# Optimization experiments

Hardware: AMD Instinct MI355X
Metric: run time of the kernel (lower is better)

Reference implementation:

```python
import jax, jax.numpy as jnp
import numpy as np

NUM_TREES = 150
ARITY = 4
DEPTH = 4
NUM_LEVELS = DEPTH + 1  # leaves (level 0) ... root (level DEPTH)
VOCAB = 10000
SUBTOK = 8
EMB_DIM = 256
HID = 256
NUM_CLASSES = 2


def _build_forest():
    # perfect ARITY-ary tree, level-order indexing; edges point child -> parent
    n = (ARITY ** (DEPTH + 1) - 1) // (ARITY - 1)  # 341
    src = np.arange(1, n)
    dst = (src - 1) // ARITY
    depth_of = np.zeros(n, dtype=np.int64)
    for j in range(1, n):
        depth_of[j] = depth_of[(j - 1) // ARITY] + 1
    level_of = DEPTH - depth_of  # leaves = 0, processed first (topo order)
    offs = np.arange(NUM_TREES) * n
    edge_src = (src[None, :] + offs[:, None]).ravel().astype(np.int32)
    edge_dst = (dst[None, :] + offs[:, None]).ravel().astype(np.int32)
    node_level = np.tile(level_of, NUM_TREES).astype(np.int32)
    graph_id = np.repeat(np.arange(NUM_TREES), n).astype(np.int32)
    leaf_mask = (node_level == 0).astype(np.int32)
    return edge_src, edge_dst, node_level, graph_id, leaf_mask, NUM_TREES * n


def setup_inputs() -> dict:
    key = jax.random.key(0)
    ks = jax.random.split(key, 16)
    es, ed, lvl, gid, lm, N = _build_forest()
    s_e = 1.0 / np.sqrt(EMB_DIM)
    s_h = 1.0 / np.sqrt(HID)
    s_f = 1.0 / np.sqrt(2 * HID)
    return {
        "node_feat1": jax.random.randint(ks[0], (N, SUBTOK), 0, VOCAB, dtype=jnp.int32),
        "node_feat2": jax.random.randint(ks[1], (N, SUBTOK), 0, VOCAB, dtype=jnp.int32),
        "emb1": jax.random.normal(ks[2], (VOCAB, EMB_DIM), jnp.float32) * 0.02,
        "emb2": jax.random.normal(ks[3], (VOCAB, EMB_DIM), jnp.float32) * 0.02,
        "W_iou1": jax.random.normal(ks[4], (EMB_DIM, 3 * HID), jnp.float32) * s_e,
        "W_iou2": jax.random.normal(ks[5], (EMB_DIM, 3 * HID), jnp.float32) * s_e,
        "U_iou1": jax.random.normal(ks[6], (HID, 3 * HID), jnp.float32) * s_h,
        "U_iou2": jax.random.normal(ks[7], (HID, 3 * HID), jnp.float32) * s_h,
        "Uf_W1": jax.random.normal(ks[8], (HID, HID), jnp.float32) * s_h,
        "Uf_b1": jnp.zeros((HID,), jnp.float32),
        "Uf_W2": jax.random.normal(ks[9], (HID, HID), jnp.float32) * s_h,
        "Uf_b2": jnp.zeros((HID,), jnp.float32),
        "b_iou1": jnp.zeros((3 * HID,), jnp.float32),
        "b_iou2": jnp.zeros((3 * HID,), jnp.float32),
        "Wf": jax.random.normal(ks[10], (2 * HID, NUM_CLASSES), jnp.float32) * s_f,
        "bf": jnp.zeros((NUM_CLASSES,), jnp.float32),
        "edge_src": jnp.asarray(es),
        "edge_dst": jnp.asarray(ed),
        "node_level": jnp.asarray(lvl),
        "graph_id": jnp.asarray(gid),
        "leaf_mask": jnp.asarray(lm),
    }


def _tree_lstm(iou0, U_iou, Uf_W, Uf_b, b_iou, edge_src, edge_dst, node_level):
    # ChildSum TreeLSTM, propagated level-by-level (leaves -> root)
    N = iou0.shape[0]
    h = jnp.zeros((N, HID), iou0.dtype)
    c = jnp.zeros((N, HID), iou0.dtype)
    for lvl in range(NUM_LEVELS):
        emask = (node_level[edge_dst] == lvl).astype(h.dtype)[:, None]  # [E,1]
        hs = h[edge_src] * emask  # children h (already computed at lower levels)
        f = jax.nn.sigmoid(hs @ Uf_W + Uf_b)  # per-edge forget gate
        h_tild = jax.ops.segment_sum(hs, edge_dst, num_segments=N)
        c_sum = jax.ops.segment_sum(f * c[edge_src] * emask, edge_dst, num_segments=N)
        has_child = jax.ops.segment_sum(emask, edge_dst, num_segments=N) > 0  # [N,1]
        # DGL semantics: reduce overwrites iou for internal nodes; leaves keep W_iou(x)*mask
        iou = jnp.where(has_child, h_tild @ U_iou, iou0) + b_iou
        i, o, u = jnp.split(iou, 3, axis=1)
        c_new = jax.nn.sigmoid(i) * jnp.tanh(u) + c_sum
        h_new = jax.nn.sigmoid(o) * jnp.tanh(c_new)
        at = (node_level == lvl)[:, None]
        h = jnp.where(at, h_new, h)
        c = jnp.where(at, c_new, c)
    return h


def _branch(node_feat, emb, W_iou, U_iou, Uf_W, Uf_b, b_iou,
            leaf_mask, edge_src, edge_dst, node_level, graph_id):
    embeds = emb[node_feat].mean(axis=1)  # subtoken mean pooling -> [N, EMB_DIM]
    iou0 = (embeds @ W_iou) * leaf_mask.astype(embeds.dtype)[:, None]
    h = _tree_lstm(iou0, U_iou, Uf_W, Uf_b, b_iou, edge_src, edge_dst, node_level)
    s = jax.ops.segment_sum(h, graph_id, num_segments=NUM_TREES)
    cnt = jax.ops.segment_sum(jnp.ones((h.shape[0],), h.dtype), graph_id, num_segments=NUM_TREES)
    return jax.nn.relu(s / cnt[:, None])  # mean graph readout + relu


def reference(node_feat1, node_feat2, emb1, emb2, W_iou1, W_iou2, U_iou1, U_iou2,
              Uf_W1, Uf_b1, Uf_W2, Uf_b2, b_iou1, b_iou2, Wf, bf,
              edge_src, edge_dst, node_level, graph_id, leaf_mask):
    m1 = _branch(node_feat1, emb1, W_iou1, U_iou1, Uf_W1, Uf_b1, b_iou1,
                 leaf_mask, edge_src, edge_dst, node_level, graph_id)
    m2 = _branch(node_feat2, emb2, W_iou2, U_iou2, Uf_W2, Uf_b2, b_iou2,
                 leaf_mask, edge_src, edge_dst, node_level, graph_id)
    logits = jax.nn.leaky_relu(jnp.concatenate([m1, m2], axis=1) @ Wf + bf, 0.01)
    return jax.nn.softmax(logits, axis=-1)
```

## Files before the change

kernel.cpp:

```cpp
#include <hip/hip_runtime.h>

#define NT 150
#define NPT 341
#define LEAF0 85
#define NL (NT*256)
#define NN (NT*NPT)
#define VOCAB 10000

typedef __attribute__((ext_vector_type(8))) short short8;
typedef __attribute__((ext_vector_type(4))) float floatx4;

__device__ __forceinline__ float sigf(float x){
  return __builtin_amdgcn_rcpf(1.0f + __expf(-x));
}
__device__ __forceinline__ float tanh_fast(float x){
  float e = __expf(2.0f*x);
  return 1.0f - 2.0f*__builtin_amdgcn_rcpf(e + 1.0f);
}
__device__ __forceinline__ float bf2f(ushort u){ union{unsigned i; float f;} v; v.i = ((unsigned)u)<<16; return v.f; }
__device__ __forceinline__ ushort f2bf(float x){ union{float f; unsigned i;} v; v.f = x; return (ushort)((v.i + 0x7fff + ((v.i>>16)&1))>>16); }

__global__ __launch_bounds__(256) void prep_k(
    const float* __restrict__ e1, const float* __restrict__ e2,
    ushort* __restrict__ E1, ushort* __restrict__ E2,
    const float* __restrict__ W1, const float* __restrict__ U1, const float* __restrict__ F1,
    const float* __restrict__ W2, const float* __restrict__ U2, const float* __restrict__ F2,
    ushort* Wt1, ushort* Ut1, ushort* Ft1, ushort* Wt2, ushort* Ut2, ushort* Ft2){
  __shared__ float T[32][33];
  int bid = blockIdx.x;
  if (bid < 5000){
    const float* s = (bid >= 2500) ? e2 : e1;
    ushort* d = (bid >= 2500) ? E2 : E1;
    size_t i = ((size_t)(bid % 2500)*256 + threadIdx.x)*4;
    float4 v = *(const float4*)&s[i];
    d[i+0]=f2bf(v.x); d[i+1]=f2bf(v.y); d[i+2]=f2bf(v.z); d[i+3]=f2bf(v.w);
    return;
  }
  int w = bid - 5000;
  int z = w / 192, rem = w % 192;
  int bx = rem % 24, by = rem / 24;
  const float* src; ushort* dst; int N;
  switch (z){
    case 0: src=W1; dst=Wt1; N=768; break;
    case 1: src=U1; dst=Ut1; N=768; break;
    case 2: src=F1; dst=Ft1; N=256; break;
    case 3: src=W2; dst=Wt2; N=768; break;
    case 4: src=U2; dst=Ut2; N=768; break;
    default: src=F2; dst=Ft2; N=256; break;
  }
  int n0 = bx*32; if (n0 >= N) return;
  int k0 = by*32;
  int nl = threadIdx.x & 31, kb = threadIdx.x >> 5;
  #pragma unroll
  for (int i=0;i<4;i++){ int kk = kb*4+i; T[kk][nl] = src[(size_t)(k0+kk)*N + n0 + nl]; }
  __syncthreads();
  #pragma unroll
  for (int i=0;i<4;i++){ int nn = kb*4+i; dst[(size_t)(n0+nn)*256 + k0 + nl] = f2bf(T[nl][nn]); }
}

__global__ __launch_bounds__(1024) void leaf_gemm(
    const int* __restrict__ f1, const int* __restrict__ f2,
    const ushort* __restrict__ E1, const ushort* __restrict__ E2,
    const ushort* __restrict__ Wt1, const float* __restrict__ b1,
    const ushort* __restrict__ Wt2, const float* __restrict__ b2,
    ushort* __restrict__ h1, ushort* __restrict__ c1,
    ushort* __restrict__ h2, ushort* __restrict__ c2){
  __shared__ __attribute__((aligned(16))) ushort As[8][64*40];
  int br = blockIdx.y;
  const int* feat = br ? f2 : f1;
  const ushort* E = br ? E2 : E1;
  const ushort* Wt = br ? Wt2 : Wt1;
  const float* biou = br ? b2 : b1;
  ushort* h = br ? h2 : h1;
  ushort* c = br ? c2 : c1;
  int tid = threadIdx.x;
  int lane = tid & 63, wav = tid >> 6, quad = lane >> 4, l15 = lane & 15;
  int rowbase = blockIdx.x*64;

  {
    int row = tid >> 4, seg = tid & 15;
    int leaf = rowbase + row;
    int tree = leaf >> 8;
    size_t node = (size_t)tree*NPT + LEAF0 + (leaf & 255);
    const int* f = feat + node*8;
    float s[16];
    #pragma unroll
    for (int q=0;q<16;q++) s[q]=0.f;
    #pragma unroll
    for (int j=0;j<8;j++){
      const ushort* rowp = E + (size_t)f[j]*256 + seg*16;
      short8 a = *(const short8*)rowp;
      short8 b = *(const short8*)(rowp+8);
      #pragma unroll
      for (int q=0;q<8;q++){ s[q]+=bf2f((ushort)a[q]); s[8+q]+=bf2f((ushort)b[q]); }
    }
    short8 o1, o2;
    #pragma unroll
    for (int q=0;q<8;q++){ o1[q]=(short)f2bf(s[q]*0.125f); o2[q]=(short)f2bf(s[8+q]*0.125f); }
    int cch = seg >> 1, off = (seg & 1)*16;
    *(short8*)&As[cch][row*40 + off]     = o1;
    *(short8*)&As[cch][row*40 + off + 8] = o2;
  }
  __syncthreads();

  floatx4 acc[3][4];
  #pragma unroll
  for (int g=0;g<3;g++)
    #pragma unroll
    for (int r=0;r<4;r++) acc[g][r] = (floatx4){0.f,0.f,0.f,0.f};

  const ushort* bp0 = Wt + (size_t)(0*256 + wav*16 + l15)*256 + quad*8;
  const ushort* bp1 = Wt + (size_t)(1*256 + wav*16 + l15)*256 + quad*8;
  const ushort* bp2 = Wt + (size_t)(2*256 + wav*16 + l15)*256 + quad*8;

  #pragma unroll
  for (int cch=0; cch<8; cch++){
    short8 b0 = *(const short8*)(bp0 + cch*32);
    short8 b1 = *(const short8*)(bp1 + cch*32);
    short8 b2 = *(const short8*)(bp2 + cch*32);
    #pragma unroll
    for (int r=0;r<4;r++){
      short8 a = *(const short8*)&As[cch][(16*r + l15)*40 + quad*8];
      acc[0][r] = __builtin_amdgcn_mfma_f32_16x16x32_bf16(a, b0, acc[0][r], 0,0,0);
      acc[1][r] = __builtin_amdgcn_mfma_f32_16x16x32_bf16(a, b1, acc[1][r], 0,0,0);
      acc[2][r] = __builtin_amdgcn_mfma_f32_16x16x32_bf16(a, b2, acc[2][r], 0,0,0);
    }
  }
  int hc = wav*16 + l15;
  float bi = biou[hc], bo = biou[256+hc], bu = biou[512+hc];
  #pragma unroll
  for (int r=0;r<4;r++){
    #pragma unroll
    for (int reg=0;reg<4;reg++){
      int leaf = rowbase + 16*r + quad*4 + reg;
      int tree = leaf >> 8;
      size_t node = (size_t)tree*NPT + LEAF0 + (leaf & 255);
      float iv = acc[0][r][reg] + bi;
      float ov = acc[1][r][reg] + bo;
      float uv = acc[2][r][reg] + bu;
      float cc = sigf(iv)*tanh_fast(uv);
      float hh = sigf(ov)*tanh_fast(cc);
      h[node*256 + hc] = f2bf(hh);
      c[node*256 + hc] = f2bf(cc);
    }
  }
}

__global__ __launch_bounds__(256) void level_k(
    const ushort* __restrict__ Ut1, const ushort* __restrict__ Ft1,
    const float* __restrict__ Ufb1, const float* __restrict__ bi1,
    const ushort* __restrict__ Ut2, const ushort* __restrict__ Ft2,
    const float* __restrict__ Ufb2, const float* __restrict__ bi2,
    ushort* __restrict__ h1, ushort* __restrict__ c1,
    ushort* __restrict__ h2, ushort* __restrict__ c2,
    int M, int shift, int base){
  __shared__ __attribute__((aligned(16))) ushort Ch[8][64*40];
  int br = blockIdx.z;
  const ushort* Ut = br ? Ut2 : Ut1;
  const ushort* Ft = br ? Ft2 : Ft1;
  const float* Ufb = br ? Ufb2 : Ufb1;
  const float* biou = br ? bi2 : bi1;
  ushort* h = br ? h2 : h1;
  ushort* c = br ? c2 : c1;
  int tid = threadIdx.x;
  int lane = tid & 63, wav = tid >> 6, quad = lane >> 4, l15 = lane & 15;
  int m0 = blockIdx.x*16, cb = blockIdx.y;
  int mask = (1<<shift)-1;

  {
    int cl = tid >> 2, q4 = tid & 3;
    int sm = m0 + (cl >> 2); if (sm > M-1) sm = M-1;
    int stree = sm >> shift, sloc = base + (sm & mask);
    const ushort* sgp = h + ((size_t)stree*NPT + 4*sloc + 1 + (cl & 3))*256 + q4*8;
    #pragma unroll
    for (int cc=0;cc<8;cc++)
      *(short8*)&Ch[cc][cl*40 + q4*8] = *(const short8*)(sgp + cc*32);
  }
  __syncthreads();

  int col = cb*64 + wav*16 + l15;
  const ushort* bfp = Ft + (size_t)col*256 + quad*8;
  const ushort* bp0 = Ut + (size_t)(0*256 + col)*256 + quad*8;
  const ushort* bp1 = Ut + (size_t)(256 + col)*256 + quad*8;
  const ushort* bp2 = Ut + (size_t)(512 + col)*256 + quad*8;

  floatx4 af[4], ai[4], ao[4], au[4];
  #pragma unroll
  for (int r=0;r<4;r++){
    af[r] = (floatx4){0.f,0.f,0.f,0.f}; ai[r] = (floatx4){0.f,0.f,0.f,0.f};
    ao[r] = (floatx4){0.f,0.f,0.f,0.f}; au[r] = (floatx4){0.f,0.f,0.f,0.f};
  }

  #pragma unroll
  for (int cc=0; cc<8; cc++){
    short8 Bf = *(const short8*)(bfp + cc*32);
    short8 Bi = *(const short8*)(bp0 + cc*32);
    short8 Bo = *(const short8*)(bp1 + cc*32);
    short8 Bu = *(const short8*)(bp2 + cc*32);
    #pragma unroll
    for (int r=0;r<4;r++){
      short8 a = *(const short8*)&Ch[cc][(16*r + l15)*40 + quad*8];
      af[r] = __builtin_amdgcn_mfma_f32_16x16x32_bf16(a, Bf, af[r], 0,0,0);
      ai[r] = __builtin_amdgcn_mfma_f32_16x16x32_bf16(a, Bi, ai[r], 0,0,0);
      ao[r] = __builtin_amdgcn_mfma_f32_16x16x32_bf16(a, Bo, ao[r], 0,0,0);
      au[r] = __builtin_amdgcn_mfma_f32_16x16x32_bf16(a, Bu, au[r], 0,0,0);
    }
  }

  float ufb = Ufb[col];
  float bI = biou[col], bO = biou[256+col], bU = biou[512+col];
  #pragma unroll
  for (int r=0;r<4;r++){
    int m = m0 + 4*r + quad;
    int mm = m < M ? m : M-1;
    int tree = mm >> shift, loc = base + (mm & mask);
    size_t ch0 = ((size_t)tree*NPT + 4*loc + 1)*256 + col;
    float cs = 0.f;
    #pragma unroll
    for (int reg=0;reg<4;reg++)
      cs += sigf(af[r][reg] + ufb) * bf2f(c[ch0 + (size_t)reg*256]);
    float iv = ai[r][0]+ai[r][1]+ai[r][2]+ai[r][3] + bI;
    float ov = ao[r][0]+ao[r][1]+ao[r][2]+ao[r][3] + bO;
    float uv = au[r][0]+au[r][1]+au[r][2]+au[r][3] + bU;
    float cn = sigf(iv)*tanh_fast(uv) + cs;
    float hn = sigf(ov)*tanh_fast(cn);
    if (m < M){
      size_t off = ((size_t)tree*NPT + loc)*256 + col;
      h[off] = f2bf(hn);
      c[off] = f2bf(cn);
    }
  }
}

__global__ __launch_bounds__(256) void readout_k(
    const ushort* __restrict__ h1, const ushort* __restrict__ h2,
    float* __restrict__ mp1, float* __restrict__ mp2){
  __shared__ float red[4][256];
  int br = blockIdx.z, part = blockIdx.y, tree = blockIdx.x;
  const ushort* h = br ? h2 : h1;
  float* mp = br ? mp2 : mp1;
  int t = threadIdx.x;
  int lane = t & 63, rg = t >> 6;
  int start = part*85;
  int cnt = (part==3) ? 86 : 85;
  const ushort* base = h + ((size_t)tree*NPT + start)*256 + lane*4;
  float s0=0.f,s1=0.f,s2=0.f,s3=0.f;
  for (int i=rg; i<cnt; i+=4){
    ushort4 v = *(const ushort4*)(base + (size_t)i*256);
    s0 += bf2f(v.x); s1 += bf2f(v.y); s2 += bf2f(v.z); s3 += bf2f(v.w);
  }
  *(float4*)&red[rg][lane*4] = make_float4(s0,s1,s2,s3);
  __syncthreads();
  float tot = red[0][t]+red[1][t]+red[2][t]+red[3][t];
  mp[((size_t)tree*4 + part)*256 + t] = tot;
}

__global__ __launch_bounds__(64) void final_k(const float* __restrict__ mp1,
    const float* __restrict__ mp2, const float* __restrict__ Wf,
    const float* __restrict__ bf, float* __restrict__ out){
  int tree = blockIdx.x; int t = threadIdx.x;
  float p0=0.f, p1=0.f;
  for (int k=t;k<512;k+=64){
    const float* mp = (k<256) ? mp1 : mp2;
    int kk = k & 255;
    size_t b0 = ((size_t)tree*4)*256 + kk;
    float s = mp[b0] + mp[b0+256] + mp[b0+512] + mp[b0+768];
    float x = fmaxf(s*(1.0f/341.0f), 0.f);
    p0 += x*Wf[k*2+0]; p1 += x*Wf[k*2+1];
  }
  #pragma unroll
  for (int off=32; off>0; off>>=1){
    p0 += __shfl_down(p0, off);
    p1 += __shfl_down(p1, off);
  }
  if (t==0){
    float l0 = p0+bf[0], l1 = p1+bf[1];
    l0 = (l0>0.f)?l0:0.01f*l0;
    l1 = (l1>0.f)?l1:0.01f*l1;
    float mx = fmaxf(l0,l1);
    float e0 = __expf(l0-mx), e1 = __expf(l1-mx);
    float inv = 1.0f/(e0+e1);
    out[tree*2+0] = e0*inv; out[tree*2+1] = e1*inv;
  }
}

extern "C" void kernel_launch(void* const* d_in, const int* in_sizes, int n_in,
                              void* d_out, int out_size, void* d_ws, size_t ws_size,
                              hipStream_t stream) {
  const int*   feat1 = (const int*)  d_in[0];
  const int*   feat2 = (const int*)  d_in[1];
  const float* emb1  = (const float*)d_in[2];
  const float* emb2  = (const float*)d_in[3];
  const float* Wiou1 = (const float*)d_in[4];
  const float* Wiou2 = (const float*)d_in[5];
  const float* Uiou1 = (const float*)d_in[6];
  const float* Uiou2 = (const float*)d_in[7];
  const float* UfW1  = (const float*)d_in[8];
  const float* Ufb1  = (const float*)d_in[9];
  const float* UfW2  = (const float*)d_in[10];
  const float* Ufb2  = (const float*)d_in[11];
  const float* biou1 = (const float*)d_in[12];
  const float* biou2 = (const float*)d_in[13];
  const float* Wf    = (const float*)d_in[14];
  const float* bfv   = (const float*)d_in[15];
  float* out = (float*)d_out;

  char* ws = (char*)d_ws;
  ushort* h1  = (ushort*)ws;  ws += (size_t)NN*256*2;
  ushort* h2  = (ushort*)ws;  ws += (size_t)NN*256*2;
  ushort* c1  = (ushort*)ws;  ws += (size_t)NN*256*2;
  ushort* c2  = (ushort*)ws;  ws += (size_t)NN*256*2;
  ushort* E1  = (ushort*)ws;  ws += (size_t)VOCAB*256*2;
  ushort* E2  = (ushort*)ws;  ws += (size_t)VOCAB*256*2;
  ushort* Wt1 = (ushort*)ws;  ws += 768*256*2;
  ushort* Ut1 = (ushort*)ws;  ws += 768*256*2;
  ushort* Ft1 = (ushort*)ws;  ws += 256*256*2;
  ushort* Wt2 = (ushort*)ws;  ws += 768*256*2;
  ushort* Ut2 = (ushort*)ws;  ws += 768*256*2;
  ushort* Ft2 = (ushort*)ws;  ws += 256*256*2;
  float*  mp1 = (float*)ws;   ws += (size_t)NT*4*256*4;
  float*  mp2 = (float*)ws;   ws += (size_t)NT*4*256*4;

  prep_k<<<dim3(6152), 256, 0, stream>>>(emb1, emb2, E1, E2,
                                         Wiou1, Uiou1, UfW1, Wiou2, Uiou2, UfW2,
                                         Wt1, Ut1, Ft1, Wt2, Ut2, Ft2);
  leaf_gemm<<<dim3(NL/64, 2), 1024, 0, stream>>>(feat1, feat2, E1, E2,
                                                 Wt1, biou1, Wt2, biou2,
                                                 h1, c1, h2, c2);

  const int lvlM[4]     = {9600, 2400, 600, 150};
  const int lvlShift[4] = {6, 4, 2, 0};
  const int lvlBase[4]  = {21, 5, 1, 0};
  for (int l=0;l<4;l++){
    int gx = (lvlM[l] + 15)/16;
    level_k<<<dim3(gx, 4, 2), 256, 0, stream>>>(Ut1, Ft1, Ufb1, biou1,
                                                Ut2, Ft2, Ufb2, biou2,
                                                h1, c1, h2, c2,
                                                lvlM[l], lvlShift[l], lvlBase[l]);
  }
  readout_k<<<dim3(NT, 4, 2), 256, 0, stream>>>(h1, h2, mp1, mp2);
  final_k<<<NT, 64, 0, stream>>>(mp1, mp2, Wf, bfv, out);
}
```

Before: 370.5 us.

## Retile leaf and level kernels to 512-thread blocks with wider column coverage

```diff
diff --git a/kernel.cpp b/kernel.cpp
--- a/kernel.cpp
+++ b/kernel.cpp
@@ -58,14 +58,14 @@
   for (int i=0;i<4;i++){ int nn = kb*4+i; dst[(size_t)(n0+nn)*256 + k0 + nl] = f2bf(T[nl][nn]); }
 }
 
-__global__ __launch_bounds__(1024) void leaf_gemm(
+__global__ __launch_bounds__(512) void leaf_gemm(
     const int* __restrict__ f1, const int* __restrict__ f2,
     const ushort* __restrict__ E1, const ushort* __restrict__ E2,
     const ushort* __restrict__ Wt1, const float* __restrict__ b1,
     const ushort* __restrict__ Wt2, const float* __restrict__ b2,
     ushort* __restrict__ h1, ushort* __restrict__ c1,
     ushort* __restrict__ h2, ushort* __restrict__ c2){
-  __shared__ __attribute__((aligned(16))) ushort As[8][64*40];
+  __shared__ __attribute__((aligned(16))) ushort As[8][32*40];
   int br = blockIdx.y;
   const int* feat = br ? f2 : f1;
   const ushort* E = br ? E2 : E1;
@@ -75,7 +75,7 @@
   ushort* c = br ? c2 : c1;
   int tid = threadIdx.x;
   int lane = tid & 63, wav = tid >> 6, quad = lane >> 4, l15 = lane & 15;
-  int rowbase = blockIdx.x*64;
+  int rowbase = blockIdx.x*32;
 
   {
     int row = tid >> 4, seg = tid & 15;
@@ -83,16 +83,26 @@
     int tree = leaf >> 8;
     size_t node = (size_t)tree*NPT + LEAF0 + (leaf & 255);
     const int* f = feat + node*8;
+    int4 fA = *(const int4*)f;
+    int4 fB = *(const int4*)(f+4);
+    int idx[8] = {fA.x, fA.y, fA.z, fA.w, fB.x, fB.y, fB.z, fB.w};
     float s[16];
     #pragma unroll
     for (int q=0;q<16;q++) s[q]=0.f;
     #pragma unroll
-    for (int j=0;j<8;j++){
-      const ushort* rowp = E + (size_t)f[j]*256 + seg*16;
-      short8 a = *(const short8*)rowp;
-      short8 b = *(const short8*)(rowp+8);
-      #pragma unroll
-      for (int q=0;q<8;q++){ s[q]+=bf2f((ushort)a[q]); s[8+q]+=bf2f((ushort)b[q]); }
+    for (int half=0; half<2; half++){
+      short8 va[4], vb[4];
+      #pragma unroll
+      for (int j=0;j<4;j++){
+        const ushort* rowp = E + (size_t)idx[half*4+j]*256 + seg*16;
+        va[j] = *(const short8*)rowp;
+        vb[j] = *(const short8*)(rowp+8);
+      }
+      #pragma unroll
+      for (int j=0;j<4;j++){
+        #pragma unroll
+        for (int q=0;q<8;q++){ s[q]+=bf2f((ushort)va[j][q]); s[8+q]+=bf2f((ushort)vb[j][q]); }
+      }
     }
     short8 o1, o2;
     #pragma unroll
@@ -103,50 +113,62 @@
   }
   __syncthreads();
 
-  floatx4 acc[3][4];
+  floatx4 acc[3][2][2];
   #pragma unroll
   for (int g=0;g<3;g++)
     #pragma unroll
-    for (int r=0;r<4;r++) acc[g][r] = (floatx4){0.f,0.f,0.f,0.f};
-
-  const ushort* bp0 = Wt + (size_t)(0*256 + wav*16 + l15)*256 + quad*8;
-  const ushort* bp1 = Wt + (size_t)(1*256 + wav*16 + l15)*256 + quad*8;
-  const ushort* bp2 = Wt + (size_t)(2*256 + wav*16 + l15)*256 + quad*8;
+    for (int cg=0;cg<2;cg++)
+      #pragma unroll
+      for (int r=0;r<2;r++) acc[g][cg][r] = (floatx4){0.f,0.f,0.f,0.f};
+
+  const ushort* bp[3][2];
+  #pragma unroll
+  for (int g=0;g<3;g++)
+    #pragma unroll
+    for (int cg=0;cg<2;cg++)
+      bp[g][cg] = Wt + (size_t)(g*256 + cg*128 + wav*16 + l15)*256 + quad*8;
 
   #pragma unroll
   for (int cch=0; cch<8; cch++){
-    short8 b0 = *(const short8*)(bp0 + cch*32);
-    short8 b1 = *(const short8*)(bp1 + cch*32);
-    short8 b2 = *(const short8*)(bp2 + cch*32);
-    #pragma unroll
-    for (int r=0;r<4;r++){
+    short8 B[3][2];
+    #pragma unroll
+    for (int g=0;g<3;g++)
+      #pragma unroll
+      for (int cg=0;cg<2;cg++) B[g][cg] = *(const short8*)(bp[g][cg] + cch*32);
+    #pragma unroll
+    for (int r=0;r<2;r++){
       short8 a = *(const short8*)&As[cch][(16*r + l15)*40 + quad*8];
-      acc[0][r] = __builtin_amdgcn_mfma_f32_16x16x32_bf16(a, b0, acc[0][r], 0,0,0);
-      acc[1][r] = __builtin_amdgcn_mfma_f32_16x16x32_bf16(a, b1, acc[1][r], 0,0,0);
-      acc[2][r] = __builtin_amdgcn_mfma_f32_16x16x32_bf16(a, b2, acc[2][r], 0,0,0);
-    }
-  }
-  int hc = wav*16 + l15;
-  float bi = biou[hc], bo = biou[256+hc], bu = biou[512+hc];
-  #pragma unroll
-  for (int r=0;r<4;r++){
-    #pragma unroll
-    for (int reg=0;reg<4;reg++){
-      int leaf = rowbase + 16*r + quad*4 + reg;
-      int tree = leaf >> 8;
-      size_t node = (size_t)tree*NPT + LEAF0 + (leaf & 255);
-      float iv = acc[0][r][reg] + bi;
-      float ov = acc[1][r][reg] + bo;
-      float uv = acc[2][r][reg] + bu;
-      float cc = sigf(iv)*tanh_fast(uv);
-      float hh = sigf(ov)*tanh_fast(cc);
-      h[node*256 + hc] = f2bf(hh);
-      c[node*256 + hc] = f2bf(cc);
-    }
-  }
-}
-
-__global__ __launch_bounds__(256) void level_k(
+      #pragma unroll
+      for (int g=0;g<3;g++)
+        #pragma unroll
+        for (int cg=0;cg<2;cg++)
+          acc[g][cg][r] = __builtin_amdgcn_mfma_f32_16x16x32_bf16(a, B[g][cg], acc[g][cg][r], 0,0,0);
+    }
+  }
+  #pragma unroll
+  for (int cg=0;cg<2;cg++){
+    int hc = cg*128 + wav*16 + l15;
+    float bi = biou[hc], bo = biou[256+hc], bu = biou[512+hc];
+    #pragma unroll
+    for (int r=0;r<2;r++){
+      #pragma unroll
+      for (int reg=0;reg<4;reg++){
+        int leaf = rowbase + 16*r + quad*4 + reg;
+        int tree = leaf >> 8;
+        size_t node = (size_t)tree*NPT + LEAF0 + (leaf & 255);
+        float iv = acc[0][cg][r][reg] + bi;
+        float ov = acc[1][cg][r][reg] + bo;
+        float uv = acc[2][cg][r][reg] + bu;
+        float cc = sigf(iv)*tanh_fast(uv);
+        float hh = sigf(ov)*tanh_fast(cc);
+        h[node*256 + hc] = f2bf(hh);
+        c[node*256 + hc] = f2bf(cc);
+      }
+    }
+  }
+}
+
+__global__ __launch_bounds__(512) void level_k(
     const ushort* __restrict__ Ut1, const ushort* __restrict__ Ft1,
     const float* __restrict__ Ufb1, const float* __restrict__ bi1,
     const ushort* __restrict__ Ut2, const ushort* __restrict__ Ft2,
@@ -164,21 +186,26 @@
   ushort* c = br ? c2 : c1;
   int tid = threadIdx.x;
   int lane = tid & 63, wav = tid >> 6, quad = lane >> 4, l15 = lane & 15;
-  int m0 = blockIdx.x*16, cb = blockIdx.y;
+  int m0 = blockIdx.x*16;
   int mask = (1<<shift)-1;
 
   {
-    int cl = tid >> 2, q4 = tid & 3;
+    int cl = tid >> 3, s8 = tid & 7;
     int sm = m0 + (cl >> 2); if (sm > M-1) sm = M-1;
     int stree = sm >> shift, sloc = base + (sm & mask);
-    const ushort* sgp = h + ((size_t)stree*NPT + 4*sloc + 1 + (cl & 3))*256 + q4*8;
-    #pragma unroll
-    for (int cc=0;cc<8;cc++)
-      *(short8*)&Ch[cc][cl*40 + q4*8] = *(const short8*)(sgp + cc*32);
+    const ushort* sgp = h + ((size_t)stree*NPT + 4*sloc + 1 + (cl & 3))*256 + s8*32;
+    short8 v0 = *(const short8*)(sgp);
+    short8 v1 = *(const short8*)(sgp+8);
+    short8 v2 = *(const short8*)(sgp+16);
+    short8 v3 = *(const short8*)(sgp+24);
+    *(short8*)&Ch[s8][cl*40 + 0]  = v0;
+    *(short8*)&Ch[s8][cl*40 + 8]  = v1;
+    *(short8*)&Ch[s8][cl*40 + 16] = v2;
+    *(short8*)&Ch[s8][cl*40 + 24] = v3;
   }
   __syncthreads();
 
-  int col = cb*64 + wav*16 + l15;
+  int col = blockIdx.y*128 + wav*16 + l15;
   const ushort* bfp = Ft + (size_t)col*256 + quad*8;
   const ushort* bp0 = Ut + (size_t)(0*256 + col)*256 + quad*8;
   const ushort* bp1 = Ut + (size_t)(256 + col)*256 + quad*8;
@@ -324,16 +351,16 @@
   prep_k<<<dim3(6152), 256, 0, stream>>>(emb1, emb2, E1, E2,
                                          Wiou1, Uiou1, UfW1, Wiou2, Uiou2, UfW2,
                                          Wt1, Ut1, Ft1, Wt2, Ut2, Ft2);
-  leaf_gemm<<<dim3(NL/64, 2), 1024, 0, stream>>>(feat1, feat2, E1, E2,
-                                                 Wt1, biou1, Wt2, biou2,
-                                                 h1, c1, h2, c2);
+  leaf_gemm<<<dim3(NL/32, 2), 512, 0, stream>>>(feat1, feat2, E1, E2,
+                                                Wt1, biou1, Wt2, biou2,
+                                                h1, c1, h2, c2);
 
   const int lvlM[4]     = {9600, 2400, 600, 150};
   const int lvlShift[4] = {6, 4, 2, 0};
   const int lvlBase[4]  = {21, 5, 1, 0};
   for (int l=0;l<4;l++){
     int gx = (lvlM[l] + 15)/16;
-    level_k<<<dim3(gx, 4, 2), 256, 0, stream>>>(Ut1, Ft1, Ufb1, biou1,
+    level_k<<<dim3(gx, 2, 2), 512, 0, stream>>>(Ut1, Ft1, Ufb1, biou1,
                                                 Ut2, Ft2, Ufb2, biou2,
                                                 h1, c1, h2, c2,
                                                 lvlM[l], lvlShift[l], lvlBase[l]);
```

Result: slower. 403.5 us (+8.9%).
